# Kernel optimization log

Hardware: AMD Instinct MI355X
Metric: run time of the kernel (lower is better)

The kernel has to match this reference:

```python
import jax, jax.numpy as jnp
import numpy as np

BN_EPS = 1e-5


def setup_inputs() -> dict:
    key = jax.random.key(0)
    k1, k2, k3, k4 = jax.random.split(key, 4)
    B, C, H, W = 16, 128, 128, 128
    x = jax.random.normal(k1, (B, C, H, W), dtype=jnp.float32)
    gamma = jax.random.normal(k2, (1,), dtype=jnp.float32)
    bn_weight = jax.random.uniform(k3, (C,), dtype=jnp.float32)
    bn_bias = jax.random.normal(k4, (C,), dtype=jnp.float32)
    return {"x": x, "gamma": gamma, "bn_weight": bn_weight, "bn_bias": bn_bias}


def reference(x, gamma, bn_weight, bn_bias):
    B, C, H, W = x.shape
    q = x.reshape(B, C, H * W)                      # proj_query: [B, C, HW]
    # energy[b, i, j] = <channel i, channel j>
    energy = jnp.einsum('bin,bjn->bij', q, q)       # [B, C, C]
    energy_new = jnp.max(energy, axis=-1, keepdims=True) - energy
    attention = jax.nn.softmax(energy_new, axis=-1)  # [B, C, C]
    out = jnp.einsum('bij,bjn->bin', attention, q)  # [B, C, HW]
    out = out.reshape(B, C, H, W)
    out = gamma * out
    # BatchNorm2d in training mode: batch statistics over (B, H, W) per channel
    mean = jnp.mean(out, axis=(0, 2, 3), keepdims=True)
    var = jnp.var(out, axis=(0, 2, 3), keepdims=True)  # biased variance
    out = (out - mean) * jax.lax.rsqrt(var + BN_EPS)
    out = out * bn_weight[None, :, None, None] + bn_bias[None, :, None, None]
    return out + x
```

## Files before the change

kernel.cpp:

```cpp
#include <hip/hip_runtime.h>

#define BB 16
#define CC 128
#define NN 16384
#define BN_EPS 1e-5f

typedef unsigned short u16;
typedef short short8 __attribute__((ext_vector_type(8)));
typedef float floatx4 __attribute__((ext_vector_type(4)));

__device__ inline float b2f(u16 u) {
    union { unsigned int i; float f; } c; c.i = ((unsigned int)u) << 16; return c.f;
}
__device__ inline u16 f2b(float f) {
    union { float f; unsigned int i; } c; c.f = f;
    unsigned int r = c.i + 0x7fffu + ((c.i >> 16) & 1u);
    return (u16)(r >> 16);
}

#define K1_LD 72
__global__ __launch_bounds__(512, 4) void k_gram(const float* __restrict__ x,
                                                 float* __restrict__ energy,
                                                 float* __restrict__ S)
{
    __shared__ u16 th[128 * K1_LD];
    __shared__ u16 tl[128 * K1_LD];
    const int rbid = blockIdx.x;
    const int xcd  = rbid & 7;
    const int li   = rbid >> 3;
    const int b    = xcd * 2 + (li >> 5);
    const int k0   = (li & 31) * 512;
    const int t    = threadIdx.x;
    const int w = t >> 6, lane = t & 63, quad = lane >> 4, colL = lane & 15;
    const int w2 = w >> 1;
    const int chf = w & 1;

    floatx4 acc[2][4];
#pragma unroll
    for (int rt = 0; rt < 2; ++rt)
#pragma unroll
        for (int ct = 0; ct < 4; ++ct) acc[rt][ct] = {0.f, 0.f, 0.f, 0.f};
    float rs[4];
#pragma unroll
    for (int it = 0; it < 4; ++it) rs[it] = 0.f;

    const float* xb = x + (size_t)b * CC * NN;
    const int rrow = t >> 4;
    const int c4   = t & 15;

    float4 v[4];
#pragma unroll
    for (int it = 0; it < 4; ++it)
        v[it] = *(const float4*)(xb + (size_t)(it * 32 + rrow) * NN + k0 + c4 * 4);

    const int arow0 = w2 * 32 + colL;
    for (int s = 0; s < 8; ++s) {
#pragma unroll
        for (int it = 0; it < 4; ++it) {
            const int row = it * 32 + rrow;
            float4 vv = v[it];
            if (s < 7)
                v[it] = *(const float4*)(xb + (size_t)row * NN + k0 + (s + 1) * 64 + c4 * 4);
            u16 h0 = f2b(vv.x), h1 = f2b(vv.y), h2 = f2b(vv.z), h3 = f2b(vv.w);
            uint2 hv, lv;
            hv.x = (unsigned)h0 | ((unsigned)h1 << 16);
            hv.y = (unsigned)h2 | ((unsigned)h3 << 16);
            lv.x = (unsigned)f2b(vv.x - b2f(h0)) | ((unsigned)f2b(vv.y - b2f(h1)) << 16);
            lv.y = (unsigned)f2b(vv.z - b2f(h2)) | ((unsigned)f2b(vv.w - b2f(h3)) << 16);
            *(uint2*)&th[row * K1_LD + c4 * 4] = hv;
            *(uint2*)&tl[row * K1_LD + c4 * 4] = lv;
            rs[it] += (vv.x + vv.y) + (vv.z + vv.w);
        }
        asm volatile("s_waitcnt lgkmcnt(0)" ::: "memory");
        __builtin_amdgcn_s_barrier();

#pragma unroll
        for (int ks2 = 0; ks2 < 2; ++ks2) {
            const int kk = ks2 * 32 + quad * 8;
            short8 a0h = *(const short8*)&th[(arow0)      * K1_LD + kk];
            short8 a0l = *(const short8*)&tl[(arow0)      * K1_LD + kk];
            short8 a1h = *(const short8*)&th[(arow0 + 16) * K1_LD + kk];
            short8 a1l = *(const short8*)&tl[(arow0 + 16) * K1_LD + kk];
#pragma unroll
            for (int ct = 0; ct < 4; ++ct) {
                const int brow = chf * 64 + ct * 16 + colL;
                short8 bh = *(const short8*)&th[brow * K1_LD + kk];
                short8 bl = *(const short8*)&tl[brow * K1_LD + kk];
                acc[0][ct] = __builtin_amdgcn_mfma_f32_16x16x32_bf16(a0h, bh, acc[0][ct], 0, 0, 0);
                acc[1][ct] = __builtin_amdgcn_mfma_f32_16x16x32_bf16(a1h, bh, acc[1][ct], 0, 0, 0);
                acc[0][ct] = __builtin_amdgcn_mfma_f32_16x16x32_bf16(a0l, bh, acc[0][ct], 0, 0, 0);
                acc[1][ct] = __builtin_amdgcn_mfma_f32_16x16x32_bf16(a1l, bh, acc[1][ct], 0, 0, 0);
                acc[0][ct] = __builtin_amdgcn_mfma_f32_16x16x32_bf16(a0h, bl, acc[0][ct], 0, 0, 0);
                acc[1][ct] = __builtin_amdgcn_mfma_f32_16x16x32_bf16(a1h, bl, acc[1][ct], 0, 0, 0);
            }
        }
        asm volatile("s_waitcnt lgkmcnt(0)" ::: "memory");
        __builtin_amdgcn_s_barrier();
    }

    float* eb = energy + b * CC * CC;
#pragma unroll
    for (int rt = 0; rt < 2; ++rt)
#pragma unroll
        for (int ct = 0; ct < 4; ++ct)
#pragma unroll
            for (int r = 0; r < 4; ++r) {
                int row = w2 * 32 + rt * 16 + quad * 4 + r;
                int col = chf * 64 + ct * 16 + colL;
                atomicAdd(&eb[row * CC + col], acc[rt][ct][r]);
            }

#pragma unroll
    for (int it = 0; it < 4; ++it) {
        float ps = rs[it];
#pragma unroll
        for (int off = 8; off > 0; off >>= 1) ps += __shfl_down(ps, off, 16);
        if (c4 == 0) atomicAdd(&S[b * CC + it * 32 + rrow], ps);
    }
}

__global__ __launch_bounds__(256) void k_soft(const float* __restrict__ energy,
                                              const float* __restrict__ S,
                                              u16* __restrict__ attb,
                                              float* __restrict__ meanacc,
                                              float* __restrict__ e2acc)
{
    const int b = blockIdx.x >> 7;
    const int i = blockIdx.x & 127;
    const int t = threadIdx.x;
    __shared__ float att[128];
    __shared__ float red[256];
    const float* E = energy + b * CC * CC;

    float e = (t < 128) ? E[i * CC + t] : 3.0e38f;
    red[t] = e; __syncthreads();
    for (int s2 = 128; s2 > 0; s2 >>= 1) { if (t < s2) red[t] = fminf(red[t], red[t + s2]); __syncthreads(); }
    float emin = red[0]; __syncthreads();

    float a = (t < 128) ? expf(emin - e) : 0.f;
    red[t] = a; __syncthreads();
    for (int s2 = 128; s2 > 0; s2 >>= 1) { if (t < s2) red[t] += red[t + s2]; __syncthreads(); }
    float Z = red[0]; __syncthreads();

    float attf = 0.f;
    if (t < 128) {
        u16 ab = f2b(a / Z);
        attf = b2f(ab);
        attb[((size_t)b * CC + i) * CC + t] = ab;
        att[t] = attf;
    }
    float mp = (t < 128) ? attf * S[b * CC + t] : 0.f;
    red[t] = mp; __syncthreads();
    for (int s2 = 128; s2 > 0; s2 >>= 1) { if (t < s2) red[t] += red[t + s2]; __syncthreads(); }
    if (t == 0) atomicAdd(&meanacc[i], red[0]);
    __syncthreads();

    const int j    = t & 127;
    const int half = t >> 7;
    const float* Ej = E + j * CC + half * 64;
    float inner = 0.f;
#pragma unroll 8
    for (int k = 0; k < 64; ++k) inner += att[half * 64 + k] * Ej[k];
    red[t] = inner; __syncthreads();
    float contrib = (t < 128) ? (red[t] + red[t + 128]) * att[t] : 0.f;
    __syncthreads();
    red[t] = contrib; __syncthreads();
    for (int s2 = 128; s2 > 0; s2 >>= 1) { if (t < s2) red[t] += red[t + s2]; __syncthreads(); }
    if (t == 0) atomicAdd(&e2acc[i], red[0]);
}

#define K3_LD 136
__global__ __launch_bounds__(256, 4) void k_out(const float* __restrict__ x,
                                                const u16* __restrict__ attb,
                                                const float* __restrict__ meanacc,
                                                const float* __restrict__ e2acc,
                                                const float* __restrict__ gamma,
                                                const float* __restrict__ bnw,
                                                const float* __restrict__ bnb,
                                                float* __restrict__ out)
{
    __shared__ u16 qT[128 * K3_LD];
    __shared__ float alpha[128];
    __shared__ float beta[128];
    const int b   = blockIdx.x >> 7;
    const int nn0 = (blockIdx.x & 127) * 128;
    const int t   = threadIdx.x;

    if (t < 128) {
        float g   = gamma[0];
        const float invBN = 1.f / (float)(BB * NN);
        float m   = g * meanacc[t] * invBN;
        float e2  = g * g * e2acc[t] * invBN;
        float var = e2 - m * m;
        float inv = rsqrtf(var + BN_EPS);
        float wv  = bnw[t];
        alpha[t] = g * wv * inv;
        beta[t]  = bnb[t] - m * wv * inv;
    }

    const float* xb = x + (size_t)b * CC * NN + nn0;
    const int n0 = (t & 31) * 4;
#pragma unroll
    for (int rep = 0; rep < 4; ++rep) {
        const int c0 = ((t >> 5) + rep * 8) * 4;
        float4 f0 = *(const float4*)(xb + (size_t)(c0 + 0) * NN + n0);
        float4 f1 = *(const float4*)(xb + (size_t)(c0 + 1) * NN + n0);
        float4 f2 = *(const float4*)(xb + (size_t)(c0 + 2) * NN + n0);
        float4 f3 = *(const float4*)(xb + (size_t)(c0 + 3) * NN + n0);
        const float fx[4] = {f0.x, f1.x, f2.x, f3.x};
        const float fy[4] = {f0.y, f1.y, f2.y, f3.y};
        const float fz[4] = {f0.z, f1.z, f2.z, f3.z};
        const float fw[4] = {f0.w, f1.w, f2.w, f3.w};
        const float* cols[4] = {fx, fy, fz, fw};
#pragma unroll
        for (int jn = 0; jn < 4; ++jn) {
            int n = n0 + jn;
            int g = ((c0 >> 3) + n) & 15;
            uint2 v;
            v.x = (unsigned)f2b(cols[jn][0]) | ((unsigned)f2b(cols[jn][1]) << 16);
            v.y = (unsigned)f2b(cols[jn][2]) | ((unsigned)f2b(cols[jn][3]) << 16);
            *(uint2*)&qT[n * K3_LD + g * 8 + (c0 & 7)] = v;
        }
    }
    __syncthreads();

    const int w = t >> 6, lane = t & 63, quad = lane >> 4, colL = lane & 15;
    const u16* ag = attb + (size_t)b * CC * CC;
    floatx4 acc[8][2];
#pragma unroll
    for (int rt = 0; rt < 8; ++rt) { acc[rt][0] = {0.f,0.f,0.f,0.f}; acc[rt][1] = {0.f,0.f,0.f,0.f}; }

#pragma unroll
    for (int ks = 0; ks < 4; ++ks) {
        const int kk = ks * 32 + quad * 8;
        const int n_a = w * 32 + colL;
        const int n_b = n_a + 16;
        short8 bf0 = *(const short8*)&qT[n_a * K3_LD + ((((kk) >> 3) + n_a) & 15) * 8];
        short8 bf1 = *(const short8*)&qT[n_b * K3_LD + ((((kk) >> 3) + n_b) & 15) * 8];
#pragma unroll
        for (int rt = 0; rt < 8; ++rt) {
            short8 af = *(const short8*)&ag[(rt * 16 + colL) * CC + kk];
            acc[rt][0] = __builtin_amdgcn_mfma_f32_16x16x32_bf16(af, bf0, acc[rt][0], 0, 0, 0);
            acc[rt][1] = __builtin_amdgcn_mfma_f32_16x16x32_bf16(af, bf1, acc[rt][1], 0, 0, 0);
        }
    }

    float* ob = out + (size_t)b * CC * NN + nn0;
#pragma unroll
    for (int rt = 0; rt < 8; ++rt)
#pragma unroll
        for (int ct = 0; ct < 2; ++ct)
#pragma unroll
            for (int r = 0; r < 4; ++r) {
                int chn = rt * 16 + quad * 4 + r;
                int nn  = w * 32 + ct * 16 + colL;
                float v = alpha[chn] * acc[rt][ct][r] + beta[chn]
                        + xb[(size_t)chn * NN + nn];
                ob[(size_t)chn * NN + nn] = v;
            }
}

extern "C" void kernel_launch(void* const* d_in, const int* in_sizes, int n_in,
                              void* d_out, int out_size, void* d_ws, size_t ws_size,
                              hipStream_t stream)
{
    const float* x     = (const float*)d_in[0];
    const float* gamma = (const float*)d_in[1];
    const float* bnw   = (const float*)d_in[2];
    const float* bnb   = (const float*)d_in[3];
    float* out = (float*)d_out;

    char* ws = (char*)d_ws;
    float* energy  = (float*)(ws);
    float* S       = (float*)(ws + 1048576);
    float* meanacc = (float*)(ws + 1056768);
    float* e2acc   = (float*)(ws + 1057280);
    u16*   attb    = (u16*)(ws + 1057792);

    hipMemsetAsync(ws, 0, 1057792, stream);
    hipLaunchKernelGGL(k_gram, dim3(512), dim3(512), 0, stream, x, energy, S);
    hipLaunchKernelGGL(k_soft, dim3(2048), dim3(256), 0, stream, energy, S, attb, meanacc, e2acc);
    hipLaunchKernelGGL(k_out,  dim3(2048), dim3(256), 0, stream, x, attb, meanacc, e2acc, gamma, bnw, bnb, out);
}
```

Measured before the change: 339.3 us.

## Replace gram atomics with partial-slab reduction, packed bf16 converts, wave-level softmax

The gram kernel now writes per-slab partial energy tiles instead of issuing float atomicAdds, and a new reduction kernel sums the 32 slabs into the energy matrix. The memset shrinks to the small accumulators. Manual bf16 rounding is replaced with the packed v_cvt_pk_bf16_f32 instruction in both the gram and output kernels. The softmax kernel is rewritten so each wavefront handles one row using shuffles instead of shared-memory tree reductions. In exchange, the partial buffer adds about 32 MB of extra traffic and one more kernel launch.

```diff
diff --git a/kernel.cpp b/kernel.cpp
--- a/kernel.cpp
+++ b/kernel.cpp
@@ -17,10 +17,15 @@
     unsigned int r = c.i + 0x7fffu + ((c.i >> 16) & 1u);
     return (u16)(r >> 16);
 }
+__device__ inline unsigned cvt_pk_bf16(float a, float b) {
+    unsigned r;
+    asm("v_cvt_pk_bf16_f32 %0, %1, %2" : "=v"(r) : "v"(a), "v"(b));
+    return r;
+}
 
 #define K1_LD 72
 __global__ __launch_bounds__(512, 4) void k_gram(const float* __restrict__ x,
-                                                 float* __restrict__ energy,
+                                                 float* __restrict__ partials,
                                                  float* __restrict__ S)
 {
     __shared__ u16 th[128 * K1_LD];
@@ -29,7 +34,8 @@
     const int xcd  = rbid & 7;
     const int li   = rbid >> 3;
     const int b    = xcd * 2 + (li >> 5);
-    const int k0   = (li & 31) * 512;
+    const int slab = li & 31;
+    const int k0   = slab * 512;
     const int t    = threadIdx.x;
     const int w = t >> 6, lane = t & 63, quad = lane >> 4, colL = lane & 15;
     const int w2 = w >> 1;
@@ -61,12 +67,15 @@
             float4 vv = v[it];
             if (s < 7)
                 v[it] = *(const float4*)(xb + (size_t)row * NN + k0 + (s + 1) * 64 + c4 * 4);
-            u16 h0 = f2b(vv.x), h1 = f2b(vv.y), h2 = f2b(vv.z), h3 = f2b(vv.w);
+            unsigned hx = cvt_pk_bf16(vv.x, vv.y);
+            unsigned hy = cvt_pk_bf16(vv.z, vv.w);
+            union { unsigned u; float f; } u0, u1, u2, u3;
+            u0.u = hx << 16; u1.u = hx & 0xffff0000u;
+            u2.u = hy << 16; u3.u = hy & 0xffff0000u;
             uint2 hv, lv;
-            hv.x = (unsigned)h0 | ((unsigned)h1 << 16);
-            hv.y = (unsigned)h2 | ((unsigned)h3 << 16);
-            lv.x = (unsigned)f2b(vv.x - b2f(h0)) | ((unsigned)f2b(vv.y - b2f(h1)) << 16);
-            lv.y = (unsigned)f2b(vv.z - b2f(h2)) | ((unsigned)f2b(vv.w - b2f(h3)) << 16);
+            hv.x = hx; hv.y = hy;
+            lv.x = cvt_pk_bf16(vv.x - u0.f, vv.y - u1.f);
+            lv.y = cvt_pk_bf16(vv.z - u2.f, vv.w - u3.f);
             *(uint2*)&th[row * K1_LD + c4 * 4] = hv;
             *(uint2*)&tl[row * K1_LD + c4 * 4] = lv;
             rs[it] += (vv.x + vv.y) + (vv.z + vv.w);
@@ -98,7 +107,7 @@
         __builtin_amdgcn_s_barrier();
     }
 
-    float* eb = energy + b * CC * CC;
+    float* pb = partials + (size_t)(b * 32 + slab) * (CC * CC);
 #pragma unroll
     for (int rt = 0; rt < 2; ++rt)
 #pragma unroll
@@ -107,7 +116,7 @@
             for (int r = 0; r < 4; ++r) {
                 int row = w2 * 32 + rt * 16 + quad * 4 + r;
                 int col = chf * 64 + ct * 16 + colL;
-                atomicAdd(&eb[row * CC + col], acc[rt][ct][r]);
+                pb[row * CC + col] = acc[rt][ct][r];
             }
 
 #pragma unroll
@@ -117,6 +126,26 @@
         for (int off = 8; off > 0; off >>= 1) ps += __shfl_down(ps, off, 16);
         if (c4 == 0) atomicAdd(&S[b * CC + it * 32 + rrow], ps);
     }
+}
+
+__global__ __launch_bounds__(256) void k_reduce(const float* __restrict__ partials,
+                                                float* __restrict__ energy)
+{
+    const size_t base = (size_t)blockIdx.x * 2048 + (size_t)threadIdx.x * 8;
+    const size_t b    = base >> 14;
+    const size_t off  = base & 16383;
+    const float* p = partials + b * (32 * (size_t)CC * CC) + off;
+    float4 s0 = {0.f, 0.f, 0.f, 0.f};
+    float4 s1 = {0.f, 0.f, 0.f, 0.f};
+#pragma unroll 8
+    for (int s = 0; s < 32; ++s) {
+        float4 a = *(const float4*)(p + (size_t)s * (CC * CC));
+        float4 c = *(const float4*)(p + (size_t)s * (CC * CC) + 4);
+        s0.x += a.x; s0.y += a.y; s0.z += a.z; s0.w += a.w;
+        s1.x += c.x; s1.y += c.y; s1.z += c.z; s1.w += c.w;
+    }
+    *(float4*)(energy + base)     = s0;
+    *(float4*)(energy + base + 4) = s1;
 }
 
 __global__ __launch_bounds__(256) void k_soft(const float* __restrict__ energy,
@@ -125,48 +154,48 @@
                                               float* __restrict__ meanacc,
                                               float* __restrict__ e2acc)
 {
-    const int b = blockIdx.x >> 7;
-    const int i = blockIdx.x & 127;
     const int t = threadIdx.x;
-    __shared__ float att[128];
-    __shared__ float red[256];
-    const float* E = energy + b * CC * CC;
-
-    float e = (t < 128) ? E[i * CC + t] : 3.0e38f;
-    red[t] = e; __syncthreads();
-    for (int s2 = 128; s2 > 0; s2 >>= 1) { if (t < s2) red[t] = fminf(red[t], red[t + s2]); __syncthreads(); }
-    float emin = red[0]; __syncthreads();
-
-    float a = (t < 128) ? expf(emin - e) : 0.f;
-    red[t] = a; __syncthreads();
-    for (int s2 = 128; s2 > 0; s2 >>= 1) { if (t < s2) red[t] += red[t + s2]; __syncthreads(); }
-    float Z = red[0]; __syncthreads();
-
-    float attf = 0.f;
-    if (t < 128) {
-        u16 ab = f2b(a / Z);
-        attf = b2f(ab);
-        attb[((size_t)b * CC + i) * CC + t] = ab;
-        att[t] = attf;
-    }
-    float mp = (t < 128) ? attf * S[b * CC + t] : 0.f;
-    red[t] = mp; __syncthreads();
-    for (int s2 = 128; s2 > 0; s2 >>= 1) { if (t < s2) red[t] += red[t + s2]; __syncthreads(); }
-    if (t == 0) atomicAdd(&meanacc[i], red[0]);
-    __syncthreads();
-
-    const int j    = t & 127;
-    const int half = t >> 7;
-    const float* Ej = E + j * CC + half * 64;
-    float inner = 0.f;
+    const int w = t >> 6, lane = t & 63;
+    const int row = blockIdx.x * 4 + w;
+    const int b = row >> 7, i = row & 127;
+    const float* E = energy + (size_t)b * CC * CC;
+
+    float2 ev = *(const float2*)&E[i * CC + lane * 2];
+    float m = fminf(ev.x, ev.y);
+#pragma unroll
+    for (int off = 1; off < 64; off <<= 1) m = fminf(m, __shfl_xor(m, off, 64));
+
+    float a0 = expf(m - ev.x);
+    float a1 = expf(m - ev.y);
+    float z = a0 + a1;
+#pragma unroll
+    for (int off = 1; off < 64; off <<= 1) z += __shfl_xor(z, off, 64);
+
+    u16 ab0 = f2b(a0 / z), ab1 = f2b(a1 / z);
+    float at0 = b2f(ab0), at1 = b2f(ab1);
+    *(unsigned*)&attb[((size_t)b * CC + i) * CC + lane * 2] =
+        (unsigned)ab0 | ((unsigned)ab1 << 16);
+
+    float2 sv = *(const float2*)&S[b * CC + lane * 2];
+    float mp = at0 * sv.x + at1 * sv.y;
+#pragma unroll
+    for (int off = 1; off < 64; off <<= 1) mp += __shfl_xor(mp, off, 64);
+    if (lane == 0) atomicAdd(&meanacc[i], mp);
+
+    float c0 = 0.f, c1 = 0.f;
 #pragma unroll 8
-    for (int k = 0; k < 64; ++k) inner += att[half * 64 + k] * Ej[k];
-    red[t] = inner; __syncthreads();
-    float contrib = (t < 128) ? (red[t] + red[t + 128]) * att[t] : 0.f;
-    __syncthreads();
-    red[t] = contrib; __syncthreads();
-    for (int s2 = 128; s2 > 0; s2 >>= 1) { if (t < s2) red[t] += red[t + s2]; __syncthreads(); }
-    if (t == 0) atomicAdd(&e2acc[i], red[0]);
+    for (int jj = 0; jj < 64; ++jj) {
+        float aj0 = __shfl(at0, jj, 64);
+        float aj1 = __shfl(at1, jj, 64);
+        float2 r0 = *(const float2*)&E[(2 * jj) * CC + lane * 2];
+        float2 r1 = *(const float2*)&E[(2 * jj + 1) * CC + lane * 2];
+        c0 += aj0 * r0.x + aj1 * r1.x;
+        c1 += aj0 * r0.y + aj1 * r1.y;
+    }
+    float e2s = at0 * c0 + at1 * c1;
+#pragma unroll
+    for (int off = 1; off < 64; off <<= 1) e2s += __shfl_xor(e2s, off, 64);
+    if (lane == 0) atomicAdd(&e2acc[i], e2s);
 }
 
 #define K3_LD 136
@@ -207,20 +236,16 @@
         float4 f1 = *(const float4*)(xb + (size_t)(c0 + 1) * NN + n0);
         float4 f2 = *(const float4*)(xb + (size_t)(c0 + 2) * NN + n0);
         float4 f3 = *(const float4*)(xb + (size_t)(c0 + 3) * NN + n0);
-        const float fx[4] = {f0.x, f1.x, f2.x, f3.x};
-        const float fy[4] = {f0.y, f1.y, f2.y, f3.y};
-        const float fz[4] = {f0.z, f1.z, f2.z, f3.z};
-        const float fw[4] = {f0.w, f1.w, f2.w, f3.w};
-        const float* cols[4] = {fx, fy, fz, fw};
-#pragma unroll
-        for (int jn = 0; jn < 4; ++jn) {
-            int n = n0 + jn;
-            int g = ((c0 >> 3) + n) & 15;
-            uint2 v;
-            v.x = (unsigned)f2b(cols[jn][0]) | ((unsigned)f2b(cols[jn][1]) << 16);
-            v.y = (unsigned)f2b(cols[jn][2]) | ((unsigned)f2b(cols[jn][3]) << 16);
-            *(uint2*)&qT[n * K3_LD + g * 8 + (c0 & 7)] = v;
-        }
+        uint2 v0, v1, v2, v3;
+        v0.x = cvt_pk_bf16(f0.x, f1.x); v0.y = cvt_pk_bf16(f2.x, f3.x);
+        v1.x = cvt_pk_bf16(f0.y, f1.y); v1.y = cvt_pk_bf16(f2.y, f3.y);
+        v2.x = cvt_pk_bf16(f0.z, f1.z); v2.y = cvt_pk_bf16(f2.z, f3.z);
+        v3.x = cvt_pk_bf16(f0.w, f1.w); v3.y = cvt_pk_bf16(f2.w, f3.w);
+        const int g0 = ((c0 >> 3) + n0) & 15;
+        *(uint2*)&qT[(n0 + 0) * K3_LD + (((g0 + 0) & 15)) * 8 + (c0 & 7)] = v0;
+        *(uint2*)&qT[(n0 + 1) * K3_LD + (((g0 + 1) & 15)) * 8 + (c0 & 7)] = v1;
+        *(uint2*)&qT[(n0 + 2) * K3_LD + (((g0 + 2) & 15)) * 8 + (c0 & 7)] = v2;
+        *(uint2*)&qT[(n0 + 3) * K3_LD + (((g0 + 3) & 15)) * 8 + (c0 & 7)] = v3;
     }
     __syncthreads();
 
@@ -271,14 +296,16 @@
     float* out = (float*)d_out;
 
     char* ws = (char*)d_ws;
-    float* energy  = (float*)(ws);
-    float* S       = (float*)(ws + 1048576);
-    float* meanacc = (float*)(ws + 1056768);
-    float* e2acc   = (float*)(ws + 1057280);
-    u16*   attb    = (u16*)(ws + 1057792);
-
-    hipMemsetAsync(ws, 0, 1057792, stream);
-    hipLaunchKernelGGL(k_gram, dim3(512), dim3(512), 0, stream, x, energy, S);
-    hipLaunchKernelGGL(k_soft, dim3(2048), dim3(256), 0, stream, energy, S, attb, meanacc, e2acc);
-    hipLaunchKernelGGL(k_out,  dim3(2048), dim3(256), 0, stream, x, attb, meanacc, e2acc, gamma, bnw, bnb, out);
-}
+    float* energy   = (float*)(ws);
+    float* S        = (float*)(ws + 1048576);
+    float* meanacc  = (float*)(ws + 1056768);
+    float* e2acc    = (float*)(ws + 1057280);
+    u16*   attb     = (u16*)(ws + 1057792);
+    float* partials = (float*)(ws + 2097152);
+
+    hipMemsetAsync(ws + 1048576, 0, 9216, stream);
+    hipLaunchKernelGGL(k_gram,   dim3(512),  dim3(512), 0, stream, x, partials, S);
+    hipLaunchKernelGGL(k_reduce, dim3(1024), dim3(256), 0, stream, partials, energy);
+    hipLaunchKernelGGL(k_soft,   dim3(512),  dim3(256), 0, stream, energy, S, attb, meanacc, e2acc);
+    hipLaunchKernelGGL(k_out,    dim3(2048), dim3(256), 0, stream, x, attb, meanacc, e2acc, gamma, bnw, bnb, out);
+}
```

After: 374.7 us. +10.4%, slower.
